# Optimization experiments

Measured on AMD Instinct MI355X. Metric: run time of the kernel, lower is better.

Reference implementation:

```python
import jax, jax.numpy as jnp
import numpy as np

N_NODES = 50000
N_EDGES = 800000
N_REL = 3
N_GRAPHS = 500
EMB = 128
IN_DIM = EMB * 3
HID = 256
N_CLASS = 10
N_SHAPE, N_COLOR, MAX_POS = 8, 8, 128


def rgcn_layer(h, src, dst, etype, W, root, b):
    """PyG RGCNConv with default aggr='mean':
    out[v] = sum_r mean_{(j->v) in E_r} h[j] @ W[r] + h[v] @ root + b
    Aggregate raw features per (dst, relation) bucket, then apply relation matmuls.
    """
    N, R = h.shape[0], W.shape[0]
    seg = dst * R + etype  # combined (node, relation) segment id
    sums = jax.ops.segment_sum(h[src], seg, num_segments=N * R)          # (N*R, d)
    cnt = jax.ops.segment_sum(jnp.ones(seg.shape, h.dtype), seg, num_segments=N * R)
    mean = (sums / jnp.maximum(cnt, 1.0)[:, None]).reshape(N, R, -1)     # (N, R, d)
    return jnp.einsum('nrd,rdh->nh', mean, W) + h @ root + b


def setup_inputs() -> dict:
    key = jax.random.key(0)
    ks = jax.random.split(key, 20)
    f32 = jnp.float32
    inp = {
        's': jax.random.randint(ks[0], (N_NODES,), 0, N_SHAPE),
        'c': jax.random.randint(ks[1], (N_NODES,), 0, N_COLOR),
        'p': jax.random.randint(ks[2], (N_NODES,), 0, MAX_POS),
        'edge_index': jax.random.randint(ks[3], (2, N_EDGES), 0, N_NODES),
        'edge_type': jax.random.randint(ks[4], (N_EDGES,), 0, N_REL),
        'batch': jnp.sort(jax.random.randint(ks[5], (N_NODES,), 0, N_GRAPHS)),
        'shape_emb': jax.random.normal(ks[6], (N_SHAPE, EMB), f32),
        'color_emb': jax.random.normal(ks[7], (N_COLOR, EMB), f32),
        'pos_emb': jax.random.normal(ks[8], (MAX_POS, EMB), f32),
        'W1': jax.random.normal(ks[9], (N_REL, IN_DIM, HID), f32) / np.sqrt(IN_DIM),
        'root1': jax.random.normal(ks[10], (IN_DIM, HID), f32) / np.sqrt(IN_DIM),
        'b1': jnp.zeros((HID,), f32),
        'W2': jax.random.normal(ks[11], (N_REL, HID, HID), f32) / np.sqrt(HID),
        'root2': jax.random.normal(ks[12], (HID, HID), f32) / np.sqrt(HID),
        'b2': jnp.zeros((HID,), f32),
        'lin_w': jax.random.normal(ks[13], (HID, N_CLASS), f32) / np.sqrt(HID),
        'lin_b': jnp.zeros((N_CLASS,), f32),
    }
    return inp


def reference(s, c, p, edge_index, edge_type, batch,
              shape_emb, color_emb, pos_emb,
              W1, root1, b1, W2, root2, b2, lin_w, lin_b):
    src, dst = edge_index[0], edge_index[1]
    h = jnp.concatenate([shape_emb[s], color_emb[c], pos_emb[p]], axis=-1)  # (N, 3*emb)
    h = jax.nn.relu(rgcn_layer(h, src, dst, edge_type, W1, root1, b1))
    h = jax.nn.relu(rgcn_layer(h, src, dst, edge_type, W2, root2, b2))
    # global_mean_pool over graphs
    gsum = jax.ops.segment_sum(h, batch, num_segments=N_GRAPHS)
    gcnt = jax.ops.segment_sum(jnp.ones((h.shape[0],), h.dtype), batch, num_segments=N_GRAPHS)
    pooled = gsum / jnp.maximum(gcnt, 1.0)[:, None]
    return pooled @ lin_w + lin_b
```

## Files before the change

### kernel.cpp

```cpp
#include <hip/hip_runtime.h>
#include <hip/hip_bf16.h>

#define NN 50000
#define NE 800000
#define NR 3
#define NG 500
#define NB (NN * NR)
#define NCLS 10
#define NCMB 8192
#define CHUNK 2048
#define NBLK ((NB + CHUNK - 1) / CHUNK)

#define P1_COMBO   196
#define P1_ZCNT    586
#define P1_ZPOOL   502
#define P1_TAB     576
#define P1_WF      1024
#define P1_TOTAL   (P1_COMBO + P1_ZCNT + P1_ZPOOL + P1_TAB + P1_WF)
#define P2_CNT     3125
#define P2_TB      768
#define P2_TOTAL   (P2_CNT + P2_TB)

typedef __hip_bfloat16 bf16;
typedef __attribute__((ext_vector_type(8))) short short8;
typedef __attribute__((ext_vector_type(4))) short shortx4;
typedef __attribute__((ext_vector_type(4))) float floatx4;

static __device__ __forceinline__ float b2f(bf16 x) { return __bfloat162float(x); }
static __device__ __forceinline__ bf16  f2b(float x) { return __float2bfloat16(x); }
static __device__ __forceinline__ float bs2f(short x) {
    return __bfloat162float(*reinterpret_cast<const bf16*>(&x));
}
static __device__ __forceinline__ short f2bs(float x) {
    bf16 b = __float2bfloat16(x);
    return *reinterpret_cast<const short*>(&b);
}
static __device__ __forceinline__ int rfl(int x) {
    return __builtin_amdgcn_readfirstlane(x);
}

__global__ __launch_bounds__(256) void prep1(const int* __restrict__ s,
                                             const int* __restrict__ c,
                                             const int* __restrict__ p,
                                             const float* __restrict__ se,
                                             const float* __restrict__ ce,
                                             const float* __restrict__ pe,
                                             const float* __restrict__ W1,
                                             const float* __restrict__ root1,
                                             const float* __restrict__ W2,
                                             const float* __restrict__ root2,
                                             int* __restrict__ combo,
                                             unsigned* __restrict__ cnt,
                                             unsigned* __restrict__ poolz,
                                             float* __restrict__ tab,
                                             bf16* __restrict__ Wf) {
    int b = blockIdx.x, t = threadIdx.x;
    if (b < P1_COMBO) {
        int n = b * 256 + t;
        if (n < NN) combo[n] = (s[n] << 10) | (c[n] << 7) | p[n];
        return;
    }
    b -= P1_COMBO;
    if (b < P1_ZCNT) {
        int i = b * 256 + t;
        if (i < NB) cnt[i] = 0u;
        return;
    }
    b -= P1_ZCNT;
    if (b < P1_ZPOOL) {
        int i = b * 256 + t;
        if (i < NG * 256 + NG) poolz[i] = 0u;
        return;
    }
    b -= P1_ZPOOL;
    if (b < P1_TAB) {
        int r = b / 144, row = b % 144;
        const float* A; int segk;
        if (row < 8)       { A = se + row * 128;        segk = 0; }
        else if (row < 16) { A = ce + (row - 8) * 128;  segk = 128; }
        else               { A = pe + (row - 16) * 128; segk = 256; }
        const float* W = (r < 3) ? (W1 + (size_t)r * 384 * 256) : root1;
        float acc = 0.f;
        for (int k = 0; k < 128; ++k)
            acc += A[k] * W[(size_t)(segk + k) * 256 + t];
        tab[((size_t)r * 144 + row) * 256 + t] = acc;
        return;
    }
    b -= P1_TAB;
    {
        int idx = b * 256 + t;
        int j     = idx & 7;
        int lane  = (idx >> 3) & 63;
        int ni    = (idx >> 9) & 3;
        int chunk = (idx >> 11) & 31;
        int colblk = idx >> 16;
        int col = colblk * 64 + ni * 16 + (lane & 15);
        int k   = chunk * 32 + (lane >> 4) * 8 + j;
        float v = (k < 768) ? W2[((size_t)(k >> 8) * 256 + (k & 255)) * 256 + col]
                            : root2[(size_t)(k - 768) * 256 + col];
        Wf[idx] = f2b(v);
    }
}

__global__ __launch_bounds__(256) void prep2(const int* __restrict__ ei,
                                             const int* __restrict__ et,
                                             int* __restrict__ cnt,
                                             const float* __restrict__ tab,
                                             const float* __restrict__ b1,
                                             bf16* __restrict__ tb2) {
    int b = blockIdx.x, t = threadIdx.x;
    if (b < P2_CNT) {
        int e = b * 256 + t;
        if (e < NE) atomicAdd(&cnt[ei[NE + e] * NR + et[e]], 1);
        return;
    }
    b -= P2_CNT;
    if (b < 256) {
        int r = b >> 6, sc = b & 63, si = sc >> 3, ci = sc & 7;
        float v = tab[((size_t)r * 144 + si) * 256 + t]
                + tab[((size_t)r * 144 + 8 + ci) * 256 + t];
        if (r == 3) v += b1[t];
        tb2[(size_t)b * 256 + t] = f2b(v);
    } else {
        int bb = b - 256;
        int r = bb >> 7, pi = bb & 127;
        tb2[(size_t)(256 + bb) * 256 + t] =
            f2b(tab[((size_t)r * 144 + 16 + pi) * 256 + t]);
    }
}

__global__ __launch_bounds__(256) void scan_block_sums(const int* __restrict__ cnt,
                                                       int* __restrict__ bsum) {
    __shared__ int sm[256];
    int b = blockIdx.x, t = threadIdx.x;
    int base = b * CHUNK + t * 8, s = 0;
#pragma unroll
    for (int j = 0; j < 8; ++j) { int i = base + j; if (i < NB) s += cnt[i]; }
    sm[t] = s; __syncthreads();
    for (int st = 128; st; st >>= 1) { if (t < st) sm[t] += sm[t + st]; __syncthreads(); }
    if (!t) bsum[b] = sm[0];
}

__global__ __launch_bounds__(256) void scan_write(const int* __restrict__ cnt,
                                                  const int* __restrict__ bsum,
                                                  int* __restrict__ off,
                                                  int* __restrict__ cursor) {
    int b = blockIdx.x, t = threadIdx.x;
    int bbase = 0;
    for (int i = 0; i < b; ++i) bbase += bsum[i];
    if (b == 0 && t == 0) {
        int tot = 0;
        for (int i = 0; i < NBLK; ++i) tot += bsum[i];
        off[NB] = tot;
    }
    int base = b * CHUNK + t * 8;
    int v[8], ts = 0;
#pragma unroll
    for (int j = 0; j < 8; ++j) { int i = base + j; v[j] = (i < NB) ? cnt[i] : 0; ts += v[j]; }
    int lane = t & 63, wv = t >> 6;
    int incl = ts;
    for (int d = 1; d < 64; d <<= 1) {
        int o = __shfl_up(incl, d, 64);
        if (lane >= d) incl += o;
    }
    __shared__ int wsum[4];
    if (lane == 63) wsum[wv] = incl;
    __syncthreads();
    int wbase = 0;
    for (int w = 0; w < wv; ++w) wbase += wsum[w];
    int run = bbase + wbase + incl - ts;
#pragma unroll
    for (int j = 0; j < 8; ++j) {
        int i = base + j;
        if (i < NB) { off[i] = run; cursor[i] = run; }
        run += v[j];
    }
}

__global__ __launch_bounds__(256) void scatter_edges(const int* __restrict__ ei,
                                                     const int* __restrict__ et,
                                                     const int* __restrict__ combo,
                                                     int* __restrict__ cursor,
                                                     unsigned* __restrict__ esc) {
    int e = blockIdx.x * 256 + threadIdx.x;
    if (e >= NE) return;
    int b = ei[NE + e] * NR + et[e];
    int pos = atomicAdd(&cursor[b], 1);
    int s = ei[e];
    esc[pos] = ((unsigned)s << 13) | (unsigned)combo[s];
}

__global__ __launch_bounds__(256) void l1_fused(const int* __restrict__ off,
                                                const unsigned* __restrict__ esc,
                                                const int* __restrict__ combo,
                                                const bf16* __restrict__ tb2,
                                                bf16* __restrict__ h1) {
    int wave = threadIdx.x >> 6, lane = threadIdx.x & 63;
    int dst = blockIdx.x * 4 + wave;
    if (dst >= NN) return;
    int half = lane >> 5, li8 = (lane & 31) * 8;
    int b0 = dst * NR;
    int o0 = off[b0], o1 = off[b0 + 1], o2 = off[b0 + 2], o3 = off[b0 + 3];
    float inv0 = (o1 > o0) ? 1.f / (float)(o1 - o0) : 0.f;
    float inv1 = (o2 > o1) ? 1.f / (float)(o2 - o1) : 0.f;
    float inv2 = (o3 > o2) ? 1.f / (float)(o3 - o2) : 0.f;
    float rootf[8] = {};
    if (half == 0) {
        int cmbD = combo[dst];
        short8 rsc = *(const short8*)(tb2 + (size_t)(192 + (cmbD >> 7)) * 256 + li8);
        short8 rp  = *(const short8*)(tb2 + (size_t)(640 + (cmbD & 127)) * 256 + li8);
#pragma unroll
        for (int i = 0; i < 8; ++i) rootf[i] = bs2f(rsc[i]) + bs2f(rp[i]);
    }
    float s[8] = {};
    int j = o0;
    for (; j + 8 <= o3; j += 8) {
        int k0 = j + half, k1 = j + 2 + half, k2 = j + 4 + half, k3 = j + 6 + half;
        unsigned e0 = esc[k0], e1 = esc[k1], e2 = esc[k2], e3 = esc[k3];
        int r0 = (k0 >= o1) + (k0 >= o2);
        int r1 = (k1 >= o1) + (k1 >= o2);
        int r2 = (k2 >= o1) + (k2 >= o2);
        int r3 = (k3 >= o1) + (k3 >= o2);
        short8 sc0 = *(const short8*)(tb2 + (size_t)(r0 * 64 + ((e0 & 8191) >> 7)) * 256 + li8);
        short8 sp0 = *(const short8*)(tb2 + (size_t)(256 + r0 * 128 + (e0 & 127)) * 256 + li8);
        short8 sc1 = *(const short8*)(tb2 + (size_t)(r1 * 64 + ((e1 & 8191) >> 7)) * 256 + li8);
        short8 sp1 = *(const short8*)(tb2 + (size_t)(256 + r1 * 128 + (e1 & 127)) * 256 + li8);
        short8 sc2 = *(const short8*)(tb2 + (size_t)(r2 * 64 + ((e2 & 8191) >> 7)) * 256 + li8);
        short8 sp2 = *(const short8*)(tb2 + (size_t)(256 + r2 * 128 + (e2 & 127)) * 256 + li8);
        short8 sc3 = *(const short8*)(tb2 + (size_t)(r3 * 64 + ((e3 & 8191) >> 7)) * 256 + li8);
        short8 sp3 = *(const short8*)(tb2 + (size_t)(256 + r3 * 128 + (e3 & 127)) * 256 + li8);
        float w0 = (k0 >= o2) ? inv2 : ((k0 >= o1) ? inv1 : inv0);
        float w1 = (k1 >= o2) ? inv2 : ((k1 >= o1) ? inv1 : inv0);
        float w2 = (k2 >= o2) ? inv2 : ((k2 >= o1) ? inv1 : inv0);
        float w3 = (k3 >= o2) ? inv2 : ((k3 >= o1) ? inv1 : inv0);
#pragma unroll
        for (int i = 0; i < 8; ++i)
            s[i] += (bs2f(sc0[i]) + bs2f(sp0[i])) * w0
                  + (bs2f(sc1[i]) + bs2f(sp1[i])) * w1
                  + (bs2f(sc2[i]) + bs2f(sp2[i])) * w2
                  + (bs2f(sc3[i]) + bs2f(sp3[i])) * w3;
    }
    for (; j + 2 <= o3; j += 2) {
        int k0 = j + half;
        unsigned e0 = esc[k0];
        int r0 = (k0 >= o1) + (k0 >= o2);
        short8 sc0 = *(const short8*)(tb2 + (size_t)(r0 * 64 + ((e0 & 8191) >> 7)) * 256 + li8);
        short8 sp0 = *(const short8*)(tb2 + (size_t)(256 + r0 * 128 + (e0 & 127)) * 256 + li8);
        float w0 = (k0 >= o2) ? inv2 : ((k0 >= o1) ? inv1 : inv0);
#pragma unroll
        for (int i = 0; i < 8; ++i) s[i] += (bs2f(sc0[i]) + bs2f(sp0[i])) * w0;
    }
    if (j < o3 && half == 0) {
        int k0 = j;
        unsigned e0 = esc[k0];
        int r0 = (k0 >= o1) + (k0 >= o2);
        short8 sc0 = *(const short8*)(tb2 + (size_t)(r0 * 64 + ((e0 & 8191) >> 7)) * 256 + li8);
        short8 sp0 = *(const short8*)(tb2 + (size_t)(256 + r0 * 128 + (e0 & 127)) * 256 + li8);
        float w0 = (k0 >= o2) ? inv2 : ((k0 >= o1) ? inv1 : inv0);
#pragma unroll
        for (int i = 0; i < 8; ++i) s[i] += (bs2f(sc0[i]) + bs2f(sp0[i])) * w0;
    }
    short8 o;
#pragma unroll
    for (int i = 0; i < 8; ++i) {
        float tot = s[i] + __shfl_xor(s[i], 32);
        o[i] = f2bs(fmaxf(rootf[i] + tot, 0.f));
    }
    if (half == 0)
        *(short8*)(h1 + (size_t)dst * 256 + li8) = o;
}

__global__ __launch_bounds__(256, 4) void agg_all(const int* __restrict__ off,
                                                  const unsigned* __restrict__ esc,
                                                  const bf16* __restrict__ h1,
                                                  bf16* __restrict__ hagg) {
    int wave = threadIdx.x >> 6, lane = threadIdx.x & 63;
    int dst = blockIdx.x * 4 + wave;
    if (dst >= NN) return;
    int l4 = lane * 4;
    int b0 = dst * NR;
    int o0 = rfl(off[b0]),     o1 = rfl(off[b0 + 1]),
        o2 = rfl(off[b0 + 2]), o3 = rfl(off[b0 + 3]);
    float s0[4] = {}, s1[4] = {}, s2[4] = {};
    int n = max(o1 - o0, max(o2 - o1, o3 - o2));
    for (int k = 0; k < n; k += 4) {
#pragma unroll
        for (int kk = 0; kk < 4; ++kk) {
            int i0 = o0 + k + kk, i1 = o1 + k + kk, i2 = o2 + k + kk;
            bool g0 = i0 < o1, g1 = i1 < o2, g2 = i2 < o3;
            unsigned e0 = esc[g0 ? i0 : 0];
            unsigned e1 = esc[g1 ? i1 : 0];
            unsigned e2 = esc[g2 ? i2 : 0];
            shortx4 v0 = *(const shortx4*)(h1 + (size_t)(g0 ? (e0 >> 13) : 0) * 256 + l4);
            shortx4 v1 = *(const shortx4*)(h1 + (size_t)(g1 ? (e1 >> 13) : 0) * 256 + l4);
            shortx4 v2 = *(const shortx4*)(h1 + (size_t)(g2 ? (e2 >> 13) : 0) * 256 + l4);
            float m0 = g0 ? 1.f : 0.f, m1 = g1 ? 1.f : 0.f, m2 = g2 ? 1.f : 0.f;
#pragma unroll
            for (int i = 0; i < 4; ++i) {
                s0[i] += bs2f(v0[i]) * m0;
                s1[i] += bs2f(v1[i]) * m1;
                s2[i] += bs2f(v2[i]) * m2;
            }
        }
    }
    float inv0 = (o1 > o0) ? 1.f / (float)(o1 - o0) : 0.f;
    float inv1 = (o2 > o1) ? 1.f / (float)(o2 - o1) : 0.f;
    float inv2 = (o3 > o2) ? 1.f / (float)(o3 - o2) : 0.f;
    shortx4 w0, w1, w2;
#pragma unroll
    for (int i = 0; i < 4; ++i) {
        w0[i] = f2bs(s0[i] * inv0);
        w1[i] = f2bs(s1[i] * inv1);
        w2[i] = f2bs(s2[i] * inv2);
    }
    bf16* hd = hagg + (size_t)dst * 768 + l4;
    *(shortx4*)(hd)       = w0;
    *(shortx4*)(hd + 256) = w1;
    *(shortx4*)(hd + 512) = w2;
}

__global__ __launch_bounds__(256) void gemm_cat(const bf16* __restrict__ hagg,
                                                const bf16* __restrict__ h1,
                                                const bf16* __restrict__ Wf,
                                                const float* __restrict__ bias,
                                                const int* __restrict__ batch,
                                                float* __restrict__ pool,
                                                float* __restrict__ gcnt) {
    __shared__ short lds[4][2][32 * 40];
    const int t = threadIdx.x;
    const int wave = t >> 6, lane = t & 63;
    const int quad = lane >> 4, l16 = lane & 15;
    const int row0 = blockIdx.x * 32;
    const int colblk = wave;
    const int rsub = lane >> 2;
    const int ksub = (lane & 3) * 8;
    short* A0 = lds[wave][0];
    short* A1 = lds[wave][1];

    const int r0 = min(row0 + rsub, NN - 1);
    const int r1 = min(row0 + 16 + rsub, NN - 1);
    const bf16* gA0 = hagg + (size_t)r0 * 768 + ksub;
    const bf16* gA1 = hagg + (size_t)r1 * 768 + ksub;
    const bf16* gH0 = h1 + (size_t)r0 * 256 + ksub;
    const bf16* gH1 = h1 + (size_t)r1 * 256 + ksub;
    const short8* bbase = (const short8*)Wf + (size_t)colblk * 32 * 4 * 64 + lane;

    auto loadA2 = [&](int k0, short8& a0, short8& a1) {
        if (k0 < 768) { a0 = *(const short8*)(gA0 + k0); a1 = *(const short8*)(gA1 + k0); }
        else          { a0 = *(const short8*)(gH0 + k0 - 768); a1 = *(const short8*)(gH1 + k0 - 768); }
    };
    auto loadB = [&](int chunk, short8* bf4) {
        const short8* bp = bbase + (size_t)chunk * 4 * 64;
#pragma unroll
        for (int ni = 0; ni < 4; ++ni) bf4[ni] = bp[ni * 64];
    };

    floatx4 acc[2][4] = {};
    short8 aE0, aE1, bE[4];
    short8 aO0, aO1, bO[4];
    loadA2(0, aE0, aE1);  loadB(0, bE);
    loadA2(32, aO0, aO1); loadB(1, bO);

#pragma unroll
    for (int i = 0; i < 32; i += 2) {
        *(short8*)&A0[rsub * 40 + ksub] = aE0;
        *(short8*)&A0[(16 + rsub) * 40 + ksub] = aE1;
        {
            short8 af0 = *(const short8*)&A0[l16 * 40 + quad * 8];
            short8 af1 = *(const short8*)&A0[(16 + l16) * 40 + quad * 8];
#pragma unroll
            for (int ni = 0; ni < 4; ++ni) {
                acc[0][ni] = __builtin_amdgcn_mfma_f32_16x16x32_bf16(af0, bE[ni], acc[0][ni], 0, 0, 0);
                acc[1][ni] = __builtin_amdgcn_mfma_f32_16x16x32_bf16(af1, bE[ni], acc[1][ni], 0, 0, 0);
            }
        }
        if (i + 2 < 32) { loadA2((i + 2) * 32, aE0, aE1); loadB(i + 2, bE); }
        *(short8*)&A1[rsub * 40 + ksub] = aO0;
        *(short8*)&A1[(16 + rsub) * 40 + ksub] = aO1;
        {
            short8 af0 = *(const short8*)&A1[l16 * 40 + quad * 8];
            short8 af1 = *(const short8*)&A1[(16 + l16) * 40 + quad * 8];
#pragma unroll
            for (int ni = 0; ni < 4; ++ni) {
                acc[0][ni] = __builtin_amdgcn_mfma_f32_16x16x32_bf16(af0, bO[ni], acc[0][ni], 0, 0, 0);
                acc[1][ni] = __builtin_amdgcn_mfma_f32_16x16x32_bf16(af1, bO[ni], acc[1][ni], 0, 0, 0);
            }
        }
        if (i + 3 < 32) { loadA2((i + 3) * 32, aO0, aO1); loadB(i + 3, bO); }
    }

    __syncthreads();
    short* st = &lds[0][0][0];
#pragma unroll
    for (int mi = 0; mi < 2; ++mi) {
#pragma unroll
        for (int ni = 0; ni < 4; ++ni) {
            int n = colblk * 64 + ni * 16 + l16;
            float bn = bias[n];
#pragma unroll
            for (int ii = 0; ii < 4; ++ii) {
                int lrow = mi * 16 + quad * 4 + ii;
                float v = (row0 + lrow < NN) ? fmaxf(acc[mi][ni][ii] + bn, 0.f) : 0.f;
                st[lrow * 260 + n] = f2bs(v);
            }
        }
    }
    __syncthreads();
    int nrows = NN - row0; if (nrows > 32) nrows = 32;
    int curg = batch[row0];
    float a = 0.f, cntf = 0.f;
    for (int rr = 0; rr < nrows; ++rr) {
        int g = batch[row0 + rr];
        if (g != curg) {
            atomicAdd(&pool[(size_t)curg * 256 + t], a);
            if (t == 0) atomicAdd(&gcnt[curg], cntf);
            a = 0.f; cntf = 0.f; curg = g;
        }
        a += bs2f(st[rr * 260 + t]);
        cntf += 1.f;
    }
    atomicAdd(&pool[(size_t)curg * 256 + t], a);
    if (t == 0) atomicAdd(&gcnt[curg], cntf);
}

__global__ __launch_bounds__(256) void final_head(const float* __restrict__ pool,
                                                  const float* __restrict__ gcnt,
                                                  const float* __restrict__ lin_w,
                                                  const float* __restrict__ lin_b,
                                                  float* __restrict__ out) {
    __shared__ float sm[256];
    int g = blockIdx.x, t = threadIdx.x;
    float inv = 1.0f / fmaxf(gcnt[g], 1.0f);
    sm[t] = pool[(size_t)g * 256 + t] * inv;
    __syncthreads();
    if (t < NCLS) {
        float s = lin_b[t];
        for (int d = 0; d < 256; ++d) s += sm[d] * lin_w[d * NCLS + t];
        out[g * NCLS + t] = s;
    }
}

extern "C" void kernel_launch(void* const* d_in, const int* in_sizes, int n_in,
                              void* d_out, int out_size, void* d_ws, size_t ws_size,
                              hipStream_t stream) {
    const int*   s_idx = (const int*)d_in[0];
    const int*   c_idx = (const int*)d_in[1];
    const int*   p_idx = (const int*)d_in[2];
    const int*   ei    = (const int*)d_in[3];
    const int*   et    = (const int*)d_in[4];
    const int*   batch = (const int*)d_in[5];
    const float* se    = (const float*)d_in[6];
    const float* ce    = (const float*)d_in[7];
    const float* pe    = (const float*)d_in[8];
    const float* W1    = (const float*)d_in[9];
    const float* root1 = (const float*)d_in[10];
    const float* b1    = (const float*)d_in[11];
    const float* W2    = (const float*)d_in[12];
    const float* root2 = (const float*)d_in[13];
    const float* b2    = (const float*)d_in[14];
    const float* lin_w = (const float*)d_in[15];
    const float* lin_b = (const float*)d_in[16];
    float* out = (float*)d_out;

    char* w = (char*)d_ws;
    size_t o = 0;
    auto alloc = [&](size_t bytes) -> void* {
        o = (o + 15) & ~(size_t)15;
        void* ptr = w + o;
        o += bytes;
        return ptr;
    };
    bf16*     hagg   = (bf16*)    alloc((size_t)NN * 768 * 2);
    bf16*     h1     = (bf16*)    alloc((size_t)NN * 256 * 2);
    bf16*     tb2    = (bf16*)    alloc((size_t)768 * 256 * 2);
    int*      combo  = (int*)     alloc((size_t)NN * 4);
    unsigned* esc    = (unsigned*)alloc((size_t)NE * 4);
    int*      cnt    = (int*)     alloc((size_t)NB * 4);
    int*      off    = (int*)     alloc((size_t)(NB + 1) * 4);
    int*      cursor = (int*)     alloc((size_t)NB * 4);
    int*      bsum   = (int*)     alloc((size_t)NBLK * 4);
    float*    tab    = (float*)   alloc((size_t)4 * 144 * 256 * 4);
    bf16*     Wf     = (bf16*)    alloc((size_t)256 * 1024 * 2);
    float*    pool   = (float*)   alloc((size_t)NG * 256 * 4);
    float*    gcnt   = (float*)   alloc((size_t)NG * 4);
    (void)ws_size;

    prep1<<<P1_TOTAL, 256, 0, stream>>>(s_idx, c_idx, p_idx, se, ce, pe,
                                        W1, root1, W2, root2,
                                        combo, (unsigned*)cnt, (unsigned*)pool, tab, Wf);
    prep2<<<P2_TOTAL, 256, 0, stream>>>(ei, et, cnt, tab, b1, tb2);
    scan_block_sums<<<NBLK, 256, 0, stream>>>(cnt, bsum);
    scan_write<<<NBLK, 256, 0, stream>>>(cnt, bsum, off, cursor);
    scatter_edges<<<(NE + 255) / 256, 256, 0, stream>>>(ei, et, combo, cursor, esc);
    l1_fused<<<(NN + 3) / 4, 256, 0, stream>>>(off, esc, combo, tb2, h1);
    agg_all<<<(NN + 3) / 4, 256, 0, stream>>>(off, esc, h1, hagg);
    gemm_cat<<<(NN + 31) / 32, 256, 0, stream>>>(hagg, h1, Wf, b2, batch, pool, gcnt);
    final_head<<<NG, 256, 0, stream>>>(pool, gcnt, lin_w, lin_b, out);
}
```

Baseline: 371.1 us.

## Gather layer-2 features from an FP8 copy and use persistent wave loops

```diff
diff --git a/kernel.cpp b/kernel.cpp
--- a/kernel.cpp
+++ b/kernel.cpp
@@ -1,5 +1,6 @@
 #include <hip/hip_runtime.h>
 #include <hip/hip_bf16.h>
+#include <hip/hip_fp8.h>
 
 #define NN 50000
 #define NE 800000
@@ -10,6 +11,7 @@
 #define NCMB 8192
 #define CHUNK 2048
 #define NBLK ((NB + CHUNK - 1) / CHUNK)
+#define PWAVES 8192
 
 #define P1_COMBO   196
 #define P1_ZCNT    586
@@ -37,6 +39,12 @@
 }
 static __device__ __forceinline__ int rfl(int x) {
     return __builtin_amdgcn_readfirstlane(x);
+}
+static __device__ __forceinline__ unsigned char f2q(float x) {
+    __hip_fp8_e4m3 q(x); return q.__x;
+}
+static __device__ __forceinline__ float q2f(unsigned char b) {
+    __hip_fp8_e4m3 q; q.__x = b; return (float)q;
 }
 
 __global__ __launch_bounds__(256) void prep1(const int* __restrict__ s,
@@ -194,129 +202,137 @@
                                                 const unsigned* __restrict__ esc,
                                                 const int* __restrict__ combo,
                                                 const bf16* __restrict__ tb2,
-                                                bf16* __restrict__ h1) {
-    int wave = threadIdx.x >> 6, lane = threadIdx.x & 63;
-    int dst = blockIdx.x * 4 + wave;
-    if (dst >= NN) return;
+                                                bf16* __restrict__ h1,
+                                                unsigned char* __restrict__ h1q) {
+    int wid = blockIdx.x * 4 + (threadIdx.x >> 6);
+    int lane = threadIdx.x & 63;
     int half = lane >> 5, li8 = (lane & 31) * 8;
-    int b0 = dst * NR;
-    int o0 = off[b0], o1 = off[b0 + 1], o2 = off[b0 + 2], o3 = off[b0 + 3];
-    float inv0 = (o1 > o0) ? 1.f / (float)(o1 - o0) : 0.f;
-    float inv1 = (o2 > o1) ? 1.f / (float)(o2 - o1) : 0.f;
-    float inv2 = (o3 > o2) ? 1.f / (float)(o3 - o2) : 0.f;
-    float rootf[8] = {};
-    if (half == 0) {
-        int cmbD = combo[dst];
-        short8 rsc = *(const short8*)(tb2 + (size_t)(192 + (cmbD >> 7)) * 256 + li8);
-        short8 rp  = *(const short8*)(tb2 + (size_t)(640 + (cmbD & 127)) * 256 + li8);
-#pragma unroll
-        for (int i = 0; i < 8; ++i) rootf[i] = bs2f(rsc[i]) + bs2f(rp[i]);
-    }
-    float s[8] = {};
-    int j = o0;
-    for (; j + 8 <= o3; j += 8) {
-        int k0 = j + half, k1 = j + 2 + half, k2 = j + 4 + half, k3 = j + 6 + half;
-        unsigned e0 = esc[k0], e1 = esc[k1], e2 = esc[k2], e3 = esc[k3];
-        int r0 = (k0 >= o1) + (k0 >= o2);
-        int r1 = (k1 >= o1) + (k1 >= o2);
-        int r2 = (k2 >= o1) + (k2 >= o2);
-        int r3 = (k3 >= o1) + (k3 >= o2);
-        short8 sc0 = *(const short8*)(tb2 + (size_t)(r0 * 64 + ((e0 & 8191) >> 7)) * 256 + li8);
-        short8 sp0 = *(const short8*)(tb2 + (size_t)(256 + r0 * 128 + (e0 & 127)) * 256 + li8);
-        short8 sc1 = *(const short8*)(tb2 + (size_t)(r1 * 64 + ((e1 & 8191) >> 7)) * 256 + li8);
-        short8 sp1 = *(const short8*)(tb2 + (size_t)(256 + r1 * 128 + (e1 & 127)) * 256 + li8);
-        short8 sc2 = *(const short8*)(tb2 + (size_t)(r2 * 64 + ((e2 & 8191) >> 7)) * 256 + li8);
-        short8 sp2 = *(const short8*)(tb2 + (size_t)(256 + r2 * 128 + (e2 & 127)) * 256 + li8);
-        short8 sc3 = *(const short8*)(tb2 + (size_t)(r3 * 64 + ((e3 & 8191) >> 7)) * 256 + li8);
-        short8 sp3 = *(const short8*)(tb2 + (size_t)(256 + r3 * 128 + (e3 & 127)) * 256 + li8);
-        float w0 = (k0 >= o2) ? inv2 : ((k0 >= o1) ? inv1 : inv0);
-        float w1 = (k1 >= o2) ? inv2 : ((k1 >= o1) ? inv1 : inv0);
-        float w2 = (k2 >= o2) ? inv2 : ((k2 >= o1) ? inv1 : inv0);
-        float w3 = (k3 >= o2) ? inv2 : ((k3 >= o1) ? inv1 : inv0);
-#pragma unroll
-        for (int i = 0; i < 8; ++i)
-            s[i] += (bs2f(sc0[i]) + bs2f(sp0[i])) * w0
-                  + (bs2f(sc1[i]) + bs2f(sp1[i])) * w1
-                  + (bs2f(sc2[i]) + bs2f(sp2[i])) * w2
-                  + (bs2f(sc3[i]) + bs2f(sp3[i])) * w3;
-    }
-    for (; j + 2 <= o3; j += 2) {
-        int k0 = j + half;
-        unsigned e0 = esc[k0];
-        int r0 = (k0 >= o1) + (k0 >= o2);
-        short8 sc0 = *(const short8*)(tb2 + (size_t)(r0 * 64 + ((e0 & 8191) >> 7)) * 256 + li8);
-        short8 sp0 = *(const short8*)(tb2 + (size_t)(256 + r0 * 128 + (e0 & 127)) * 256 + li8);
-        float w0 = (k0 >= o2) ? inv2 : ((k0 >= o1) ? inv1 : inv0);
-#pragma unroll
-        for (int i = 0; i < 8; ++i) s[i] += (bs2f(sc0[i]) + bs2f(sp0[i])) * w0;
-    }
-    if (j < o3 && half == 0) {
-        int k0 = j;
-        unsigned e0 = esc[k0];
-        int r0 = (k0 >= o1) + (k0 >= o2);
-        short8 sc0 = *(const short8*)(tb2 + (size_t)(r0 * 64 + ((e0 & 8191) >> 7)) * 256 + li8);
-        short8 sp0 = *(const short8*)(tb2 + (size_t)(256 + r0 * 128 + (e0 & 127)) * 256 + li8);
-        float w0 = (k0 >= o2) ? inv2 : ((k0 >= o1) ? inv1 : inv0);
-#pragma unroll
-        for (int i = 0; i < 8; ++i) s[i] += (bs2f(sc0[i]) + bs2f(sp0[i])) * w0;
-    }
-    short8 o;
-#pragma unroll
-    for (int i = 0; i < 8; ++i) {
-        float tot = s[i] + __shfl_xor(s[i], 32);
-        o[i] = f2bs(fmaxf(rootf[i] + tot, 0.f));
-    }
-    if (half == 0)
-        *(short8*)(h1 + (size_t)dst * 256 + li8) = o;
+    for (int dst = wid; dst < NN; dst += PWAVES) {
+        int b0 = dst * NR;
+        int o0 = off[b0], o1 = off[b0 + 1], o2 = off[b0 + 2], o3 = off[b0 + 3];
+        float inv0 = (o1 > o0) ? 1.f / (float)(o1 - o0) : 0.f;
+        float inv1 = (o2 > o1) ? 1.f / (float)(o2 - o1) : 0.f;
+        float inv2 = (o3 > o2) ? 1.f / (float)(o3 - o2) : 0.f;
+        float rootf[8] = {};
+        if (half == 0) {
+            int cmbD = combo[dst];
+            short8 rsc = *(const short8*)(tb2 + (size_t)(192 + (cmbD >> 7)) * 256 + li8);
+            short8 rp  = *(const short8*)(tb2 + (size_t)(640 + (cmbD & 127)) * 256 + li8);
+#pragma unroll
+            for (int i = 0; i < 8; ++i) rootf[i] = bs2f(rsc[i]) + bs2f(rp[i]);
+        }
+        float s[8] = {};
+        int j = o0;
+        for (; j + 8 <= o3; j += 8) {
+            int k0 = j + half, k1 = j + 2 + half, k2 = j + 4 + half, k3 = j + 6 + half;
+            unsigned e0 = esc[k0], e1 = esc[k1], e2 = esc[k2], e3 = esc[k3];
+            int r0 = (k0 >= o1) + (k0 >= o2);
+            int r1 = (k1 >= o1) + (k1 >= o2);
+            int r2 = (k2 >= o1) + (k2 >= o2);
+            int r3 = (k3 >= o1) + (k3 >= o2);
+            short8 sc0 = *(const short8*)(tb2 + (size_t)(r0 * 64 + ((e0 & 8191) >> 7)) * 256 + li8);
+            short8 sp0 = *(const short8*)(tb2 + (size_t)(256 + r0 * 128 + (e0 & 127)) * 256 + li8);
+            short8 sc1 = *(const short8*)(tb2 + (size_t)(r1 * 64 + ((e1 & 8191) >> 7)) * 256 + li8);
+            short8 sp1 = *(const short8*)(tb2 + (size_t)(256 + r1 * 128 + (e1 & 127)) * 256 + li8);
+            short8 sc2 = *(const short8*)(tb2 + (size_t)(r2 * 64 + ((e2 & 8191) >> 7)) * 256 + li8);
+            short8 sp2 = *(const short8*)(tb2 + (size_t)(256 + r2 * 128 + (e2 & 127)) * 256 + li8);
+            short8 sc3 = *(const short8*)(tb2 + (size_t)(r3 * 64 + ((e3 & 8191) >> 7)) * 256 + li8);
+            short8 sp3 = *(const short8*)(tb2 + (size_t)(256 + r3 * 128 + (e3 & 127)) * 256 + li8);
+            float w0 = (k0 >= o2) ? inv2 : ((k0 >= o1) ? inv1 : inv0);
+            float w1 = (k1 >= o2) ? inv2 : ((k1 >= o1) ? inv1 : inv0);
+            float w2 = (k2 >= o2) ? inv2 : ((k2 >= o1) ? inv1 : inv0);
+            float w3 = (k3 >= o2) ? inv2 : ((k3 >= o1) ? inv1 : inv0);
+#pragma unroll
+            for (int i = 0; i < 8; ++i)
+                s[i] += (bs2f(sc0[i]) + bs2f(sp0[i])) * w0
+                      + (bs2f(sc1[i]) + bs2f(sp1[i])) * w1
+                      + (bs2f(sc2[i]) + bs2f(sp2[i])) * w2
+                      + (bs2f(sc3[i]) + bs2f(sp3[i])) * w3;
+        }
+        for (; j + 2 <= o3; j += 2) {
+            int k0 = j + half;
+            unsigned e0 = esc[k0];
+            int r0 = (k0 >= o1) + (k0 >= o2);
+            short8 sc0 = *(const short8*)(tb2 + (size_t)(r0 * 64 + ((e0 & 8191) >> 7)) * 256 + li8);
+            short8 sp0 = *(const short8*)(tb2 + (size_t)(256 + r0 * 128 + (e0 & 127)) * 256 + li8);
+            float w0 = (k0 >= o2) ? inv2 : ((k0 >= o1) ? inv1 : inv0);
+#pragma unroll
+            for (int i = 0; i < 8; ++i) s[i] += (bs2f(sc0[i]) + bs2f(sp0[i])) * w0;
+        }
+        if (j < o3 && half == 0) {
+            int k0 = j;
+            unsigned e0 = esc[k0];
+            int r0 = (k0 >= o1) + (k0 >= o2);
+            short8 sc0 = *(const short8*)(tb2 + (size_t)(r0 * 64 + ((e0 & 8191) >> 7)) * 256 + li8);
+            short8 sp0 = *(const short8*)(tb2 + (size_t)(256 + r0 * 128 + (e0 & 127)) * 256 + li8);
+            float w0 = (k0 >= o2) ? inv2 : ((k0 >= o1) ? inv1 : inv0);
+#pragma unroll
+            for (int i = 0; i < 8; ++i) s[i] += (bs2f(sc0[i]) + bs2f(sp0[i])) * w0;
+        }
+        short8 o;
+        union { unsigned char b[8]; unsigned long long u; } pk;
+#pragma unroll
+        for (int i = 0; i < 8; ++i) {
+            float tot = s[i] + __shfl_xor(s[i], 32);
+            float v = fmaxf(rootf[i] + tot, 0.f);
+            o[i] = f2bs(v);
+            pk.b[i] = f2q(v);
+        }
+        if (half == 0) {
+            *(short8*)(h1 + (size_t)dst * 256 + li8) = o;
+            *(unsigned long long*)(h1q + (size_t)dst * 256 + li8) = pk.u;
+        }
+    }
 }
 
 __global__ __launch_bounds__(256, 4) void agg_all(const int* __restrict__ off,
                                                   const unsigned* __restrict__ esc,
-                                                  const bf16* __restrict__ h1,
+                                                  const unsigned char* __restrict__ h1q,
                                                   bf16* __restrict__ hagg) {
-    int wave = threadIdx.x >> 6, lane = threadIdx.x & 63;
-    int dst = blockIdx.x * 4 + wave;
-    if (dst >= NN) return;
+    int wid = blockIdx.x * 4 + (threadIdx.x >> 6);
+    int lane = threadIdx.x & 63;
     int l4 = lane * 4;
-    int b0 = dst * NR;
-    int o0 = rfl(off[b0]),     o1 = rfl(off[b0 + 1]),
-        o2 = rfl(off[b0 + 2]), o3 = rfl(off[b0 + 3]);
-    float s0[4] = {}, s1[4] = {}, s2[4] = {};
-    int n = max(o1 - o0, max(o2 - o1, o3 - o2));
-    for (int k = 0; k < n; k += 4) {
-#pragma unroll
-        for (int kk = 0; kk < 4; ++kk) {
-            int i0 = o0 + k + kk, i1 = o1 + k + kk, i2 = o2 + k + kk;
-            bool g0 = i0 < o1, g1 = i1 < o2, g2 = i2 < o3;
-            unsigned e0 = esc[g0 ? i0 : 0];
-            unsigned e1 = esc[g1 ? i1 : 0];
-            unsigned e2 = esc[g2 ? i2 : 0];
-            shortx4 v0 = *(const shortx4*)(h1 + (size_t)(g0 ? (e0 >> 13) : 0) * 256 + l4);
-            shortx4 v1 = *(const shortx4*)(h1 + (size_t)(g1 ? (e1 >> 13) : 0) * 256 + l4);
-            shortx4 v2 = *(const shortx4*)(h1 + (size_t)(g2 ? (e2 >> 13) : 0) * 256 + l4);
-            float m0 = g0 ? 1.f : 0.f, m1 = g1 ? 1.f : 0.f, m2 = g2 ? 1.f : 0.f;
-#pragma unroll
-            for (int i = 0; i < 4; ++i) {
-                s0[i] += bs2f(v0[i]) * m0;
-                s1[i] += bs2f(v1[i]) * m1;
-                s2[i] += bs2f(v2[i]) * m2;
+    for (int dst = wid; dst < NN; dst += PWAVES) {
+        int b0 = dst * NR;
+        int o0 = rfl(off[b0]),     o1 = rfl(off[b0 + 1]),
+            o2 = rfl(off[b0 + 2]), o3 = rfl(off[b0 + 3]);
+        float s0[4] = {}, s1[4] = {}, s2[4] = {};
+        int n = max(o1 - o0, max(o2 - o1, o3 - o2));
+        for (int k = 0; k < n; k += 4) {
+#pragma unroll
+            for (int kk = 0; kk < 4; ++kk) {
+                int i0 = o0 + k + kk, i1 = o1 + k + kk, i2 = o2 + k + kk;
+                bool g0 = i0 < o1, g1 = i1 < o2, g2 = i2 < o3;
+                unsigned e0 = esc[g0 ? i0 : 0];
+                unsigned e1 = esc[g1 ? i1 : 0];
+                unsigned e2 = esc[g2 ? i2 : 0];
+                unsigned q0 = *(const unsigned*)(h1q + (size_t)(g0 ? (e0 >> 13) : 0) * 256 + l4);
+                unsigned q1 = *(const unsigned*)(h1q + (size_t)(g1 ? (e1 >> 13) : 0) * 256 + l4);
+                unsigned q2v = *(const unsigned*)(h1q + (size_t)(g2 ? (e2 >> 13) : 0) * 256 + l4);
+                float m0 = g0 ? 1.f : 0.f, m1 = g1 ? 1.f : 0.f, m2 = g2 ? 1.f : 0.f;
+#pragma unroll
+                for (int i = 0; i < 4; ++i) {
+                    s0[i] += q2f((q0  >> (8 * i)) & 0xff) * m0;
+                    s1[i] += q2f((q1  >> (8 * i)) & 0xff) * m1;
+                    s2[i] += q2f((q2v >> (8 * i)) & 0xff) * m2;
+                }
             }
         }
-    }
-    float inv0 = (o1 > o0) ? 1.f / (float)(o1 - o0) : 0.f;
-    float inv1 = (o2 > o1) ? 1.f / (float)(o2 - o1) : 0.f;
-    float inv2 = (o3 > o2) ? 1.f / (float)(o3 - o2) : 0.f;
-    shortx4 w0, w1, w2;
-#pragma unroll
-    for (int i = 0; i < 4; ++i) {
-        w0[i] = f2bs(s0[i] * inv0);
-        w1[i] = f2bs(s1[i] * inv1);
-        w2[i] = f2bs(s2[i] * inv2);
-    }
-    bf16* hd = hagg + (size_t)dst * 768 + l4;
-    *(shortx4*)(hd)       = w0;
-    *(shortx4*)(hd + 256) = w1;
-    *(shortx4*)(hd + 512) = w2;
+        float inv0 = (o1 > o0) ? 1.f / (float)(o1 - o0) : 0.f;
+        float inv1 = (o2 > o1) ? 1.f / (float)(o2 - o1) : 0.f;
+        float inv2 = (o3 > o2) ? 1.f / (float)(o3 - o2) : 0.f;
+        shortx4 w0, w1, w2;
+#pragma unroll
+        for (int i = 0; i < 4; ++i) {
+            w0[i] = f2bs(s0[i] * inv0);
+            w1[i] = f2bs(s1[i] * inv1);
+            w2[i] = f2bs(s2[i] * inv2);
+        }
+        bf16* hd = hagg + (size_t)dst * 768 + l4;
+        *(shortx4*)(hd)       = w0;
+        *(shortx4*)(hd + 256) = w1;
+        *(shortx4*)(hd + 512) = w2;
+    }
 }
 
 __global__ __launch_bounds__(256) void gemm_cat(const bf16* __restrict__ hagg,
@@ -472,6 +488,7 @@
     };
     bf16*     hagg   = (bf16*)    alloc((size_t)NN * 768 * 2);
     bf16*     h1     = (bf16*)    alloc((size_t)NN * 256 * 2);
+    unsigned char* h1q = (unsigned char*)alloc((size_t)NN * 256);
     bf16*     tb2    = (bf16*)    alloc((size_t)768 * 256 * 2);
     int*      combo  = (int*)     alloc((size_t)NN * 4);
     unsigned* esc    = (unsigned*)alloc((size_t)NE * 4);
@@ -492,8 +509,8 @@
     scan_block_sums<<<NBLK, 256, 0, stream>>>(cnt, bsum);
     scan_write<<<NBLK, 256, 0, stream>>>(cnt, bsum, off, cursor);
     scatter_edges<<<(NE + 255) / 256, 256, 0, stream>>>(ei, et, combo, cursor, esc);
-    l1_fused<<<(NN + 3) / 4, 256, 0, stream>>>(off, esc, combo, tb2, h1);
-    agg_all<<<(NN + 3) / 4, 256, 0, stream>>>(off, esc, h1, hagg);
+    l1_fused<<<PWAVES / 4, 256, 0, stream>>>(off, esc, combo, tb2, h1, h1q);
+    agg_all<<<PWAVES / 4, 256, 0, stream>>>(off, esc, h1q, hagg);
     gemm_cat<<<(NN + 31) / 32, 256, 0, stream>>>(hagg, h1, Wf, b2, batch, pool, gcnt);
     final_head<<<NG, 256, 0, stream>>>(pool, gcnt, lin_w, lin_b, out);
 }
```

New measurement: 373.3 us. Within noise of the previous version (+0.6%).
